# Kernel tuning notes

Hardware: AMD Instinct MI355X
Metric: run time of the kernel (lower is better)

Reference implementation:

```python
import jax, jax.numpy as jnp
import numpy as np

NB_STEPS = 300  # quadrature steps hard-coded in EmbeddingNet.__init__
B, D, C = 2048, 128, 64  # batch, in_main(=in_embedding), out_embedding


def _glorot(key, shape):
    fan_in, fan_out = shape
    lim = (6.0 / (fan_in + fan_out)) ** 0.5
    return jax.random.uniform(key, shape, jnp.float32, -lim, lim)


def setup_inputs() -> dict:
    key = jax.random.key(0)
    ks = jax.random.split(key, 9)
    x = jax.random.uniform(ks[0], (B, D), jnp.float32)
    # embedding net: D -> 200 -> 200 -> C (ReLU after every layer)
    W1 = _glorot(ks[1], (D, 200)); b1 = jnp.zeros((200,), jnp.float32)
    W2 = _glorot(ks[2], (200, 200)); b2 = jnp.zeros((200,), jnp.float32)
    W3 = _glorot(ks[3], (200, C)); b3 = jnp.zeros((C,), jnp.float32)
    # UMNN integrand net: (D + C) -> 100 -> 100 -> 100 -> D, positive output via ELU+1
    U1 = _glorot(ks[4], (D + C, 100)); c1 = jnp.zeros((100,), jnp.float32)
    U2 = _glorot(ks[5], (100, 100)); c2 = jnp.zeros((100,), jnp.float32)
    U3 = _glorot(ks[6], (100, 100)); c3 = jnp.zeros((100,), jnp.float32)
    U4 = _glorot(ks[7], (100, D)); c4 = jnp.zeros((D,), jnp.float32)
    return {"x": x, "W1": W1, "b1": b1, "W2": W2, "b2": b2, "W3": W3, "b3": b3,
            "U1": U1, "c1": c1, "U2": U2, "c2": c2, "U3": U3, "c3": c3,
            "U4": U4, "c4": c4}


def _forward(x, W1, b1, W2, b2, W3, b3, U1, c1, U2, c2, U3, c3, U4, c4):
    # conditioning embedding h = embedding_net(x)
    h = jax.nn.relu(x @ W1 + b1)
    h = jax.nn.relu(h @ W2 + b2)
    h = jax.nn.relu(h @ W3 + b3)                                   # (B, C)
    # UMNN: F(x,h) = int_0^1 f(t*x, h) . x dt, f > 0 via ELU+1 => monotone in each x_d.
    # All NB_STEPS quadrature points evaluated as one batched GEMM (the 'fast' form
    # of the original Python-level 300-step loop). Midpoint rule on (0,1).
    t = (jnp.arange(NB_STEPS, dtype=x.dtype) + 0.5) / NB_STEPS     # (T,)
    X = t[None, :, None] * x[:, None, :]                           # (B, T, D) points on path 0 -> x
    Hc = jnp.broadcast_to(h[:, None, :], (x.shape[0], NB_STEPS, h.shape[1]))
    z = jnp.concatenate([X, Hc], axis=-1)                          # (B, T, D+C)
    a = jax.nn.relu(z @ U1 + c1)
    a = jax.nn.relu(a @ U2 + c2)
    a = jax.nn.relu(a @ U3 + c3)
    f = jax.nn.elu(a @ U4 + c4) + 1.0                              # (B, T, D), strictly positive
    F = jnp.einsum('btd,bd->b', f, x) / NB_STEPS                   # line-integral quadrature
    return jax.nn.sigmoid(F)[:, None]                              # (B, 1)


def reference(x, W1, b1, W2, b2, W3, b3, U1, c1, U2, c2, U3, c3, U4, c4):
    return _forward(x, W1, b1, W2, b2, W3, b3, U1, c1, U2, c2, U3, c3, U4, c4)
```

## Files before the change

### kernel.cpp

```cpp
#include <hip/hip_runtime.h>

typedef __attribute__((ext_vector_type(8))) short bf16x8;
typedef __attribute__((ext_vector_type(4))) float f32x4;
typedef __attribute__((ext_vector_type(16))) float f32x16;
typedef int v2i __attribute__((ext_vector_type(2)));

union U4B { unsigned u[4]; bf16x8 v; };

__device__ __forceinline__ unsigned short f2bf(float f) {
    union { float f; unsigned u; } v; v.f = f;
    unsigned r = v.u + 0x7fffu + ((v.u >> 16) & 1u);
    return (unsigned short)(r >> 16);
}

__device__ __forceinline__ unsigned pkbf(float a, float b) {
    unsigned r;
    asm("v_cvt_pk_bf16_f32 %0, %1, %2" : "=v"(r) : "v"(a), "v"(b));
    return r;
}

__device__ __forceinline__ f32x16 zero16() {
    f32x16 v;
#pragma unroll
    for (int i = 0; i < 16; ++i) v[i] = 0.f;
    return v;
}

#define BATCH   2048
#define TSTEPS  300
#define ROWS_PB 4
#define WT_OFF  0
#define G_OFF   98304
#define E_OFF   1146880
#define OFF_X   98304
#define OFF_G   100352
#define OFF_E   102400
#define OFF_P   104448
#define SMEM_SZ 104480

__global__ __launch_bounds__(256) void prep_kernel(
    const float* __restrict__ U2, const float* __restrict__ c2,
    const float* __restrict__ U3, const float* __restrict__ c3,
    const float* __restrict__ U4, const float* __restrict__ c4,
    unsigned char* __restrict__ ws)
{
    int idx = blockIdx.x * 256 + threadIdx.x;
    for (int i = idx; i < 3 * 128 * 128; i += 48 * 256) {
        int m = i >> 14;
        int r = i & 16383;
        int n = r >> 7;
        int k = r & 127;
        float v = 0.f;
        if (m == 2) {
            if (k < 100)       v = U4[k * 128 + n];
            else if (k == 100) v = c4[n];
        } else {
            const float* U = (m == 0) ? U2 : U3;
            const float* c = (m == 0) ? c2 : c3;
            if (n < 100) {
                if (k < 100)       v = U[k * 100 + n];
                else if (k == 100) v = c[n];
            } else if (n == 100 && k == 100) {
                v = 1.f;
            }
        }
        *(unsigned short*)(ws + WT_OFF + m * 32768 + n * 256 + k * 2) = f2bf(v);
    }
}

__global__ __launch_bounds__(256) void embed_kernel(
    const float* __restrict__ x,
    const float* __restrict__ W1, const float* __restrict__ b1,
    const float* __restrict__ W2, const float* __restrict__ b2,
    const float* __restrict__ W3, const float* __restrict__ b3,
    const float* __restrict__ U1, const float* __restrict__ c1,
    float* __restrict__ g_out, float* __restrict__ e_out)
{
    __shared__ float xs[4][128];
    __shared__ float h1[4][200];
    __shared__ float h2[4][200];
    __shared__ float h3[4][64];
    const int tid = threadIdx.x;
    const int b0 = blockIdx.x * 4;

    for (int i = tid; i < 4 * 128; i += 256) {
        int r = i >> 7, d = i & 127;
        xs[r][d] = x[(b0 + r) * 128 + d];
    }
    __syncthreads();

    const int j = tid;
    if (j < 200) {
        float acc[4];
#pragma unroll
        for (int r = 0; r < 4; ++r) acc[r] = b1[j];
        for (int d = 0; d < 128; ++d) {
            float w = W1[d * 200 + j];
#pragma unroll
            for (int r = 0; r < 4; ++r) acc[r] += xs[r][d] * w;
        }
#pragma unroll
        for (int r = 0; r < 4; ++r) h1[r][j] = fmaxf(acc[r], 0.f);
    }
    __syncthreads();
    if (j < 200) {
        float acc[4];
#pragma unroll
        for (int r = 0; r < 4; ++r) acc[r] = b2[j];
        for (int d = 0; d < 200; ++d) {
            float w = W2[d * 200 + j];
#pragma unroll
            for (int r = 0; r < 4; ++r) acc[r] += h1[r][d] * w;
        }
#pragma unroll
        for (int r = 0; r < 4; ++r) h2[r][j] = fmaxf(acc[r], 0.f);
    }
    __syncthreads();
    if (j < 64) {
        float acc[4];
#pragma unroll
        for (int r = 0; r < 4; ++r) acc[r] = b3[j];
        for (int d = 0; d < 200; ++d) {
            float w = W3[d * 64 + j];
#pragma unroll
            for (int r = 0; r < 4; ++r) acc[r] += h2[r][d] * w;
        }
#pragma unroll
        for (int r = 0; r < 4; ++r) h3[r][j] = fmaxf(acc[r], 0.f);
    }
    __syncthreads();
    if (j < 128) {
        float ga[4], ea[4];
#pragma unroll
        for (int r = 0; r < 4; ++r) { ga[r] = 0.f; ea[r] = 0.f; }
        if (j < 100) {
            for (int d = 0; d < 128; ++d) {
                float w = U1[d * 100 + j];
#pragma unroll
                for (int r = 0; r < 4; ++r) ga[r] += xs[r][d] * w;
            }
#pragma unroll
            for (int r = 0; r < 4; ++r) ea[r] = c1[j];
            for (int c = 0; c < 64; ++c) {
                float w = U1[(128 + c) * 100 + j];
#pragma unroll
                for (int r = 0; r < 4; ++r) ea[r] += h3[r][c] * w;
            }
        } else if (j == 100) {
#pragma unroll
            for (int r = 0; r < 4; ++r) ea[r] = 1.f;
        }
#pragma unroll
        for (int r = 0; r < 4; ++r) {
            g_out[(b0 + r) * 128 + j] = ga[r];
            e_out[(b0 + r) * 128 + j] = ea[r];
        }
    }
}

__global__ __launch_bounds__(512, 1) void umnn_main(
    const float* __restrict__ x,
    const float* __restrict__ ws_g, const float* __restrict__ ws_e,
    const unsigned char* __restrict__ ws, float* __restrict__ out)
{
    extern __shared__ char sm[];
    float* sX = (float*)(sm + OFF_X);
    float* sG = (float*)(sm + OFF_G);
    float* sE = (float*)(sm + OFF_E);
    float* sP = (float*)(sm + OFF_P);
    const int tid = threadIdx.x;
    const int lane = tid & 63, wid = tid >> 6;
    const int l31 = lane & 31, hi = lane >> 5;
    const int b4 = blockIdx.x * ROWS_PB;

    {
        const uint4* src = (const uint4*)(ws + WT_OFF);
        for (int ci = tid; ci < 6144; ci += 512) {
            int m = ci >> 11, wi = ci & 2047, n = wi >> 4, part = wi & 15;
            uint4 v = src[ci];
            *(uint4*)(sm + m * 32768 + n * 256 + ((part * 16) ^ ((n & 7) << 4))) = v;
        }
        {
            int i = tid;
            int r = i >> 7, d = i & 127;
            sX[i] = x[(b4 + r) * 128 + d];
            sG[i] = ws_g[(b4 + r) * 128 + d];
            sE[i] = ws_e[(b4 + r) * 128 + d];
        }
    }
    __syncthreads();

    const int row = wid >> 1, half = wid & 1;
    const float* gR = sG + row * 128;
    const float* eR = sE + row * 128;
    const float* xR = sX + row * 128;
    const int sw = (l31 & 7) << 4;
    const char* wB2 = sm;
    const char* wB3 = sm + 32768;
    const char* wB4 = sm + 65536;

    float sumF = 0.f;

#pragma unroll 1
    for (int s = 0; s < 5; ++s) {
        const int t = half * 160 + s * 32 + l31;
        const float tt = ((float)t + 0.5f) * (1.f / 300.f);

        bf16x8 B[7];
#pragma unroll
        for (int ks = 0; ks < 7; ++ks) {
            const int k0 = ks * 16 + hi * 8;
            f32x4 g0 = *(const f32x4*)(gR + k0);
            f32x4 g1 = *(const f32x4*)(gR + k0 + 4);
            f32x4 e0 = *(const f32x4*)(eR + k0);
            f32x4 e1 = *(const f32x4*)(eR + k0 + 4);
            float a0 = fmaxf(fmaf(tt, g0[0], e0[0]), 0.f);
            float a1 = fmaxf(fmaf(tt, g0[1], e0[1]), 0.f);
            float a2 = fmaxf(fmaf(tt, g0[2], e0[2]), 0.f);
            float a3 = fmaxf(fmaf(tt, g0[3], e0[3]), 0.f);
            float a4 = fmaxf(fmaf(tt, g1[0], e1[0]), 0.f);
            float a5 = fmaxf(fmaf(tt, g1[1], e1[1]), 0.f);
            float a6 = fmaxf(fmaf(tt, g1[2], e1[2]), 0.f);
            float a7 = fmaxf(fmaf(tt, g1[3], e1[3]), 0.f);
            U4B u;
            u.u[0] = pkbf(a0, a1); u.u[1] = pkbf(a2, a3);
            u.u[2] = pkbf(a4, a5); u.u[3] = pkbf(a6, a7);
            B[ks] = u.v;
        }

#pragma unroll
        for (int L = 0; L < 2; ++L) {
            const char* wb = (L == 0) ? wB2 : wB3;
            f32x16 acc[4];
#pragma unroll
            for (int f = 0; f < 4; ++f) acc[f] = zero16();
#pragma unroll
            for (int ks = 0; ks < 7; ++ks) {
                const int ko = ks * 32 + hi * 16;
#pragma unroll
                for (int f = 0; f < 4; ++f) {
                    bf16x8 a = *(const bf16x8*)(wb + (32 * f + l31) * 256 + (ko ^ sw));
                    acc[f] = __builtin_amdgcn_mfma_f32_32x32x16_bf16(a, B[ks], acc[f], 0, 0, 0);
                }
            }
#pragma unroll
            for (int f = 0; f < 4; ++f) {
#pragma unroll
                for (int r = 0; r < 16; ++r) acc[f][r] = fmaxf(acc[f][r], 0.f);
                {
                    unsigned u  = pkbf(acc[f][0], acc[f][1]);
                    unsigned u2 = pkbf(acc[f][2], acc[f][3]);
                    unsigned v  = pkbf(acc[f][4], acc[f][5]);
                    unsigned v2 = pkbf(acc[f][6], acc[f][7]);
                    v2i r1 = __builtin_amdgcn_permlane32_swap(u, v, false, false);
                    v2i r2 = __builtin_amdgcn_permlane32_swap(u2, v2, false, false);
                    U4B b; b.u[0] = r1.x; b.u[1] = r2.x; b.u[2] = r1.y; b.u[3] = r2.y;
                    B[2 * f] = b.v;
                }
                if (f < 3) {
                    unsigned u  = pkbf(acc[f][8],  acc[f][9]);
                    unsigned u2 = pkbf(acc[f][10], acc[f][11]);
                    unsigned v  = pkbf(acc[f][12], acc[f][13]);
                    unsigned v2 = pkbf(acc[f][14], acc[f][15]);
                    v2i r1 = __builtin_amdgcn_permlane32_swap(u, v, false, false);
                    v2i r2 = __builtin_amdgcn_permlane32_swap(u2, v2, false, false);
                    U4B b; b.u[0] = r1.x; b.u[1] = r2.x; b.u[2] = r1.y; b.u[3] = r2.y;
                    B[2 * f + 1] = b.v;
                }
            }
        }

        float sdot = 0.f;
#pragma unroll
        for (int f = 0; f < 4; ++f) {
            f32x16 acc = zero16();
#pragma unroll
            for (int ks = 0; ks < 7; ++ks) {
                const int ko = ks * 32 + hi * 16;
                bf16x8 a = *(const bf16x8*)(wB4 + (32 * f + l31) * 256 + (ko ^ sw));
                acc = __builtin_amdgcn_mfma_f32_32x32x16_bf16(a, B[ks], acc, 0, 0, 0);
            }
#pragma unroll
            for (int q = 0; q < 4; ++q) {
                const int n0 = f * 32 + q * 8 + hi * 4;
                f32x4 xv = *(const f32x4*)(xR + n0);
#pragma unroll
                for (int i = 0; i < 4; ++i) {
                    float p = acc[q * 4 + i];
                    float fv = (p > 0.f) ? (p + 1.f) : __expf(p);
                    sdot = fmaf(fv, xv[i], sdot);
                }
            }
        }
        if (t < TSTEPS) sumF += sdot;
    }

#pragma unroll
    for (int off = 32; off >= 1; off >>= 1) sumF += __shfl_xor(sumF, off);
    if (lane == 0) sP[wid] = sumF;
    __syncthreads();
    if (tid < ROWS_PB) {
        float F = (sP[tid * 2] + sP[tid * 2 + 1]) * (1.f / 300.f);
        out[b4 + tid] = 1.f / (1.f + __expf(-F));
    }
}

extern "C" void kernel_launch(void* const* d_in, const int* in_sizes, int n_in,
                              void* d_out, int out_size, void* d_ws, size_t ws_size,
                              hipStream_t stream)
{
    const float* x  = (const float*)d_in[0];
    const float* W1 = (const float*)d_in[1];
    const float* b1 = (const float*)d_in[2];
    const float* W2 = (const float*)d_in[3];
    const float* b2 = (const float*)d_in[4];
    const float* W3 = (const float*)d_in[5];
    const float* b3 = (const float*)d_in[6];
    const float* U1 = (const float*)d_in[7];
    const float* c1 = (const float*)d_in[8];
    const float* U2 = (const float*)d_in[9];
    const float* c2 = (const float*)d_in[10];
    const float* U3 = (const float*)d_in[11];
    const float* c3 = (const float*)d_in[12];
    const float* U4 = (const float*)d_in[13];
    const float* c4 = (const float*)d_in[14];
    float* out = (float*)d_out;
    unsigned char* ws = (unsigned char*)d_ws;

    prep_kernel<<<48, 256, 0, stream>>>(U2, c2, U3, c3, U4, c4, ws);
    embed_kernel<<<BATCH / 4, 256, 0, stream>>>(x, W1, b1, W2, b2, W3, b3, U1, c1,
                                                (float*)(ws + G_OFF), (float*)(ws + E_OFF));
    hipFuncSetAttribute((const void*)umnn_main,
                        hipFuncAttributeMaxDynamicSharedMemorySize, SMEM_SZ);
    umnn_main<<<BATCH / ROWS_PB, 512, SMEM_SZ, stream>>>(
        x, (const float*)(ws + G_OFF), (const float*)(ws + E_OFF), ws, out);
}
```

Baseline: 168.3 us.

## Move embedding net to bf16 MFMA and process eight rows per main block

Replaces the scalar per-row embedding kernel with a 16-block MFMA version. It stages bf16 swizzled weights in LDS, runs all four small GEMMs on matrix cores, and writes g/e as bf16. The main UMNN kernel now handles 8 batch rows per 1024-thread block, so each LDS weight load is shared by more rows, and it uses a wider XOR swizzle. Risks: the embedding runs on only 16 blocks, bf16 intermediates lose precision, and launch_bounds(1024,2) may force a low VGPR budget and cause spills.

New measurement: 240.2 us. 42.7% more time.

```diff
diff --git a/kernel.cpp b/kernel.cpp
--- a/kernel.cpp
+++ b/kernel.cpp
@@ -12,13 +12,24 @@
     unsigned r = v.u + 0x7fffu + ((v.u >> 16) & 1u);
     return (unsigned short)(r >> 16);
 }
-
+__device__ __forceinline__ float bf2f(unsigned short s) {
+    union { unsigned u; float f; } v; v.u = ((unsigned)s) << 16; return v.f;
+}
 __device__ __forceinline__ unsigned pkbf(float a, float b) {
     unsigned r;
     asm("v_cvt_pk_bf16_f32 %0, %1, %2" : "=v"(r) : "v"(a), "v"(b));
     return r;
 }
-
+__device__ __forceinline__ bf16x8 packhalf(const f32x16& a, int base) {
+    unsigned u  = pkbf(a[base + 0], a[base + 1]);
+    unsigned u2 = pkbf(a[base + 2], a[base + 3]);
+    unsigned v  = pkbf(a[base + 4], a[base + 5]);
+    unsigned v2 = pkbf(a[base + 6], a[base + 7]);
+    v2i r1 = __builtin_amdgcn_permlane32_swap(u, v, false, false);
+    v2i r2 = __builtin_amdgcn_permlane32_swap(u2, v2, false, false);
+    U4B b; b.u[0] = r1.x; b.u[1] = r2.x; b.u[2] = r1.y; b.u[3] = r2.y;
+    return b.v;
+}
 __device__ __forceinline__ f32x16 zero16() {
     f32x16 v;
 #pragma unroll
@@ -28,15 +39,20 @@
 
 #define BATCH   2048
 #define TSTEPS  300
-#define ROWS_PB 4
-#define WT_OFF  0
+#define ROWS_PB 8
+#define WM_OFF  0
 #define G_OFF   98304
-#define E_OFF   1146880
+#define E_OFF   622592
 #define OFF_X   98304
-#define OFF_G   100352
-#define OFF_E   102400
-#define OFF_P   104448
-#define SMEM_SZ 104480
+#define OFF_G   102400
+#define OFF_E   106496
+#define OFF_P   110592
+#define SMEM_M  110656
+#define EB1     114688
+#define EB2     115584
+#define EB3     116480
+#define EC1     116736
+#define SMEM_E  117248
 
 __global__ __launch_bounds__(256) void prep_kernel(
     const float* __restrict__ U2, const float* __restrict__ c2,
@@ -45,7 +61,7 @@
     unsigned char* __restrict__ ws)
 {
     int idx = blockIdx.x * 256 + threadIdx.x;
-    for (int i = idx; i < 3 * 128 * 128; i += 48 * 256) {
+    for (int i = idx; i < 3 * 128 * 128; i += 24 * 256) {
         int m = i >> 14;
         int r = i & 16383;
         int n = r >> 7;
@@ -64,103 +80,202 @@
                 v = 1.f;
             }
         }
-        *(unsigned short*)(ws + WT_OFF + m * 32768 + n * 256 + k * 2) = f2bf(v);
-    }
-}
-
-__global__ __launch_bounds__(256) void embed_kernel(
+        *(unsigned short*)(ws + WM_OFF + m * 32768 + n * 256 + k * 2) = f2bf(v);
+    }
+}
+
+__global__ __launch_bounds__(256, 1) void embed2(
     const float* __restrict__ x,
     const float* __restrict__ W1, const float* __restrict__ b1,
     const float* __restrict__ W2, const float* __restrict__ b2,
     const float* __restrict__ W3, const float* __restrict__ b3,
     const float* __restrict__ U1, const float* __restrict__ c1,
-    float* __restrict__ g_out, float* __restrict__ e_out)
+    unsigned char* __restrict__ ws)
 {
-    __shared__ float xs[4][128];
-    __shared__ float h1[4][200];
-    __shared__ float h2[4][200];
-    __shared__ float h3[4][64];
+    extern __shared__ char sm[];
     const int tid = threadIdx.x;
-    const int b0 = blockIdx.x * 4;
-
-    for (int i = tid; i < 4 * 128; i += 256) {
-        int r = i >> 7, d = i & 127;
-        xs[r][d] = x[(b0 + r) * 128 + d];
-    }
-    __syncthreads();
-
-    const int j = tid;
-    if (j < 200) {
-        float acc[4];
-#pragma unroll
-        for (int r = 0; r < 4; ++r) acc[r] = b1[j];
-        for (int d = 0; d < 128; ++d) {
-            float w = W1[d * 200 + j];
-#pragma unroll
-            for (int r = 0; r < 4; ++r) acc[r] += xs[r][d] * w;
-        }
-#pragma unroll
-        for (int r = 0; r < 4; ++r) h1[r][j] = fmaxf(acc[r], 0.f);
-    }
-    __syncthreads();
-    if (j < 200) {
-        float acc[4];
-#pragma unroll
-        for (int r = 0; r < 4; ++r) acc[r] = b2[j];
-        for (int d = 0; d < 200; ++d) {
-            float w = W2[d * 200 + j];
-#pragma unroll
-            for (int r = 0; r < 4; ++r) acc[r] += h1[r][d] * w;
-        }
-#pragma unroll
-        for (int r = 0; r < 4; ++r) h2[r][j] = fmaxf(acc[r], 0.f);
-    }
-    __syncthreads();
-    if (j < 64) {
-        float acc[4];
-#pragma unroll
-        for (int r = 0; r < 4; ++r) acc[r] = b3[j];
-        for (int d = 0; d < 200; ++d) {
-            float w = W3[d * 64 + j];
-#pragma unroll
-            for (int r = 0; r < 4; ++r) acc[r] += h2[r][d] * w;
-        }
-#pragma unroll
-        for (int r = 0; r < 4; ++r) h3[r][j] = fmaxf(acc[r], 0.f);
-    }
-    __syncthreads();
-    if (j < 128) {
-        float ga[4], ea[4];
-#pragma unroll
-        for (int r = 0; r < 4; ++r) { ga[r] = 0.f; ea[r] = 0.f; }
-        if (j < 100) {
-            for (int d = 0; d < 128; ++d) {
-                float w = U1[d * 100 + j];
-#pragma unroll
-                for (int r = 0; r < 4; ++r) ga[r] += xs[r][d] * w;
-            }
-#pragma unroll
-            for (int r = 0; r < 4; ++r) ea[r] = c1[j];
-            for (int c = 0; c < 64; ++c) {
-                float w = U1[(128 + c) * 100 + j];
-#pragma unroll
-                for (int r = 0; r < 4; ++r) ea[r] += h3[r][c] * w;
-            }
-        } else if (j == 100) {
-#pragma unroll
-            for (int r = 0; r < 4; ++r) ea[r] = 1.f;
-        }
-#pragma unroll
-        for (int r = 0; r < 4; ++r) {
-            g_out[(b0 + r) * 128 + j] = ga[r];
-            e_out[(b0 + r) * 128 + j] = ea[r];
-        }
-    }
-}
-
-__global__ __launch_bounds__(512, 1) void umnn_main(
+    const int lane = tid & 63, wid = tid >> 6;
+    const int l31 = lane & 31, hi = lane >> 5;
+    const int brow = blockIdx.x * 128 + wid * 32 + l31;
+    const int sw8 = (l31 & 15) << 4;
+    const int sw9 = (l31 & 31) << 4;
+
+    for (int i = tid; i < 224; i += 256) ((float*)(sm + EB1))[i] = (i < 200) ? b1[i] : 0.f;
+    for (int i = tid; i < 224; i += 256) ((float*)(sm + EB2))[i] = (i < 200) ? b2[i] : 0.f;
+    if (tid < 64)  ((float*)(sm + EB3))[tid] = b3[tid];
+    if (tid < 128) ((float*)(sm + EC1))[tid] = (tid < 100) ? c1[tid] : 0.f;
+
+    for (int i = tid; i < 224 * 128; i += 256) {
+        int n = i >> 7, k = i & 127;
+        float v = (n < 200) ? W1[k * 200 + n] : 0.f;
+        *(unsigned short*)(sm + n * 256 + ((k * 2) ^ ((n & 15) << 4))) = f2bf(v);
+    }
+    for (int i = tid; i < 128 * 128; i += 256) {
+        int n = i >> 7, k = i & 127;
+        float v = (n < 100) ? U1[k * 100 + n] : 0.f;
+        *(unsigned short*)(sm + 57344 + n * 256 + ((k * 2) ^ ((n & 15) << 4))) = f2bf(v);
+    }
+    __syncthreads();
+
+    bf16x8 Bx[8];
+    {
+        const float* xr = x + brow * 128;
+#pragma unroll
+        for (int ks = 0; ks < 8; ++ks) {
+            const int k0 = ks * 16 + hi * 8;
+            f32x4 a = *(const f32x4*)(xr + k0);
+            f32x4 b = *(const f32x4*)(xr + k0 + 4);
+            U4B u;
+            u.u[0] = pkbf(a[0], a[1]); u.u[1] = pkbf(a[2], a[3]);
+            u.u[2] = pkbf(b[0], b[1]); u.u[3] = pkbf(b[2], b[3]);
+            Bx[ks] = u.v;
+        }
+    }
+
+    unsigned short* g16 = (unsigned short*)(ws + G_OFF);
+    unsigned short* e16 = (unsigned short*)(ws + E_OFF);
+
+    {
+        f32x16 ag[4];
+#pragma unroll
+        for (int f = 0; f < 4; ++f) ag[f] = zero16();
+#pragma unroll
+        for (int ks = 0; ks < 8; ++ks)
+#pragma unroll
+            for (int f = 0; f < 4; ++f) {
+                bf16x8 a = *(const bf16x8*)(sm + 57344 + (32 * f + l31) * 256 + ((ks * 32 + hi * 16) ^ sw8));
+                ag[f] = __builtin_amdgcn_mfma_f32_32x32x16_bf16(a, Bx[ks], ag[f], 0, 0, 0);
+            }
+#pragma unroll
+        for (int f = 0; f < 4; ++f)
+#pragma unroll
+            for (int r = 0; r < 16; r += 2) {
+                int n = 32 * f + (r & 3) + 8 * (r >> 2) + 4 * hi;
+                *(unsigned*)(g16 + brow * 128 + n) = pkbf(ag[f][r], ag[f][r + 1]);
+            }
+    }
+
+    bf16x8 Bh[13];
+    {
+        f32x16 acc[7];
+#pragma unroll
+        for (int f = 0; f < 7; ++f)
+#pragma unroll
+            for (int r = 0; r < 16; ++r)
+                acc[f][r] = ((float*)(sm + EB1))[32 * f + (r & 3) + 8 * (r >> 2) + 4 * hi];
+#pragma unroll
+        for (int ks = 0; ks < 8; ++ks)
+#pragma unroll
+            for (int f = 0; f < 7; ++f) {
+                bf16x8 a = *(const bf16x8*)(sm + (32 * f + l31) * 256 + ((ks * 32 + hi * 16) ^ sw8));
+                acc[f] = __builtin_amdgcn_mfma_f32_32x32x16_bf16(a, Bx[ks], acc[f], 0, 0, 0);
+            }
+#pragma unroll
+        for (int f = 0; f < 7; ++f) {
+#pragma unroll
+            for (int r = 0; r < 16; ++r) acc[f][r] = fmaxf(acc[f][r], 0.f);
+            Bh[2 * f] = packhalf(acc[f], 0);
+            if (f < 6) Bh[2 * f + 1] = packhalf(acc[f], 8);
+        }
+    }
+    __syncthreads();
+
+    for (int i = tid; i < 224 * 256; i += 256) {
+        int n = i >> 8, k = i & 255;
+        float v = (n < 200 && k < 200) ? W2[k * 200 + n] : 0.f;
+        *(unsigned short*)(sm + n * 512 + ((k * 2) ^ ((n & 31) << 4))) = f2bf(v);
+    }
+    __syncthreads();
+
+    bf16x8 Bh2[13];
+    {
+        f32x16 acc[7];
+#pragma unroll
+        for (int f = 0; f < 7; ++f)
+#pragma unroll
+            for (int r = 0; r < 16; ++r)
+                acc[f][r] = ((float*)(sm + EB2))[32 * f + (r & 3) + 8 * (r >> 2) + 4 * hi];
+#pragma unroll
+        for (int ks = 0; ks < 13; ++ks)
+#pragma unroll
+            for (int f = 0; f < 7; ++f) {
+                bf16x8 a = *(const bf16x8*)(sm + (32 * f + l31) * 512 + ((ks * 32 + hi * 16) ^ sw9));
+                acc[f] = __builtin_amdgcn_mfma_f32_32x32x16_bf16(a, Bh[ks], acc[f], 0, 0, 0);
+            }
+#pragma unroll
+        for (int f = 0; f < 7; ++f) {
+#pragma unroll
+            for (int r = 0; r < 16; ++r) acc[f][r] = fmaxf(acc[f][r], 0.f);
+            Bh2[2 * f] = packhalf(acc[f], 0);
+            if (f < 6) Bh2[2 * f + 1] = packhalf(acc[f], 8);
+        }
+    }
+    __syncthreads();
+
+    for (int i = tid; i < 64 * 256; i += 256) {
+        int n = i >> 8, k = i & 255;
+        float v = (k < 200) ? W3[k * 64 + n] : 0.f;
+        *(unsigned short*)(sm + n * 512 + ((k * 2) ^ ((n & 31) << 4))) = f2bf(v);
+    }
+    for (int i = tid; i < 128 * 128; i += 256) {
+        int n = i >> 7, k = i & 127;
+        float v = (n < 100 && k < 64) ? U1[(128 + k) * 100 + n] : 0.f;
+        *(unsigned short*)(sm + 32768 + n * 256 + ((k * 2) ^ ((n & 15) << 4))) = f2bf(v);
+    }
+    __syncthreads();
+
+    bf16x8 B4[4];
+    {
+        f32x16 acc[2];
+#pragma unroll
+        for (int f = 0; f < 2; ++f)
+#pragma unroll
+            for (int r = 0; r < 16; ++r)
+                acc[f][r] = ((float*)(sm + EB3))[32 * f + (r & 3) + 8 * (r >> 2) + 4 * hi];
+#pragma unroll
+        for (int ks = 0; ks < 13; ++ks)
+#pragma unroll
+            for (int f = 0; f < 2; ++f) {
+                bf16x8 a = *(const bf16x8*)(sm + (32 * f + l31) * 512 + ((ks * 32 + hi * 16) ^ sw9));
+                acc[f] = __builtin_amdgcn_mfma_f32_32x32x16_bf16(a, Bh2[ks], acc[f], 0, 0, 0);
+            }
+#pragma unroll
+        for (int f = 0; f < 2; ++f) {
+#pragma unroll
+            for (int r = 0; r < 16; ++r) acc[f][r] = fmaxf(acc[f][r], 0.f);
+            B4[2 * f]     = packhalf(acc[f], 0);
+            B4[2 * f + 1] = packhalf(acc[f], 8);
+        }
+    }
+
+    {
+        f32x16 ae[4];
+#pragma unroll
+        for (int f = 0; f < 4; ++f)
+#pragma unroll
+            for (int r = 0; r < 16; ++r)
+                ae[f][r] = ((float*)(sm + EC1))[32 * f + (r & 3) + 8 * (r >> 2) + 4 * hi];
+#pragma unroll
+        for (int ks = 0; ks < 4; ++ks)
+#pragma unroll
+            for (int f = 0; f < 4; ++f) {
+                bf16x8 a = *(const bf16x8*)(sm + 32768 + (32 * f + l31) * 256 + ((ks * 32 + hi * 16) ^ sw8));
+                ae[f] = __builtin_amdgcn_mfma_f32_32x32x16_bf16(a, B4[ks], ae[f], 0, 0, 0);
+            }
+#pragma unroll
+        for (int f = 0; f < 4; ++f)
+#pragma unroll
+            for (int r = 0; r < 16; r += 2) {
+                int n = 32 * f + (r & 3) + 8 * (r >> 2) + 4 * hi;
+                float v0 = ae[f][r], v1 = ae[f][r + 1];
+                if (n == 100) v0 = 1.f;
+                *(unsigned*)(e16 + brow * 128 + n) = pkbf(v0, v1);
+            }
+    }
+}
+
+__global__ __launch_bounds__(1024, 2) void umnn_main(
     const float* __restrict__ x,
-    const float* __restrict__ ws_g, const float* __restrict__ ws_e,
     const unsigned char* __restrict__ ws, float* __restrict__ out)
 {
     extern __shared__ char sm[];
@@ -171,21 +286,22 @@
     const int tid = threadIdx.x;
     const int lane = tid & 63, wid = tid >> 6;
     const int l31 = lane & 31, hi = lane >> 5;
-    const int b4 = blockIdx.x * ROWS_PB;
-
-    {
-        const uint4* src = (const uint4*)(ws + WT_OFF);
-        for (int ci = tid; ci < 6144; ci += 512) {
+    const int b8 = blockIdx.x * ROWS_PB;
+
+    {
+        const uint4* src = (const uint4*)(ws + WM_OFF);
+        for (int ci = tid; ci < 6144; ci += 1024) {
             int m = ci >> 11, wi = ci & 2047, n = wi >> 4, part = wi & 15;
             uint4 v = src[ci];
-            *(uint4*)(sm + m * 32768 + n * 256 + ((part * 16) ^ ((n & 7) << 4))) = v;
-        }
+            *(uint4*)(sm + m * 32768 + n * 256 + ((part * 16) ^ ((n & 15) << 4))) = v;
+        }
+        const unsigned short* g16 = (const unsigned short*)(ws + G_OFF);
+        const unsigned short* e16 = (const unsigned short*)(ws + E_OFF);
         {
-            int i = tid;
-            int r = i >> 7, d = i & 127;
-            sX[i] = x[(b4 + r) * 128 + d];
-            sG[i] = ws_g[(b4 + r) * 128 + d];
-            sE[i] = ws_e[(b4 + r) * 128 + d];
+            int r = tid >> 7, d = tid & 127;
+            sX[tid] = x[(b8 + r) * 128 + d];
+            sG[tid] = bf2f(g16[(b8 + r) * 128 + d]);
+            sE[tid] = bf2f(e16[(b8 + r) * 128 + d]);
         }
     }
     __syncthreads();
@@ -194,7 +310,7 @@
     const float* gR = sG + row * 128;
     const float* eR = sE + row * 128;
     const float* xR = sX + row * 128;
-    const int sw = (l31 & 7) << 4;
+    const int sw = (l31 & 15) << 4;
     const char* wB2 = sm;
     const char* wB3 = sm + 32768;
     const char* wB4 = sm + 65536;
@@ -247,26 +363,8 @@
             for (int f = 0; f < 4; ++f) {
 #pragma unroll
                 for (int r = 0; r < 16; ++r) acc[f][r] = fmaxf(acc[f][r], 0.f);
-                {
-                    unsigned u  = pkbf(acc[f][0], acc[f][1]);
-                    unsigned u2 = pkbf(acc[f][2], acc[f][3]);
-                    unsigned v  = pkbf(acc[f][4], acc[f][5]);
-                    unsigned v2 = pkbf(acc[f][6], acc[f][7]);
-                    v2i r1 = __builtin_amdgcn_permlane32_swap(u, v, false, false);
-                    v2i r2 = __builtin_amdgcn_permlane32_swap(u2, v2, false, false);
-                    U4B b; b.u[0] = r1.x; b.u[1] = r2.x; b.u[2] = r1.y; b.u[3] = r2.y;
-                    B[2 * f] = b.v;
-                }
-                if (f < 3) {
-                    unsigned u  = pkbf(acc[f][8],  acc[f][9]);
-                    unsigned u2 = pkbf(acc[f][10], acc[f][11]);
-                    unsigned v  = pkbf(acc[f][12], acc[f][13]);
-                    unsigned v2 = pkbf(acc[f][14], acc[f][15]);
-                    v2i r1 = __builtin_amdgcn_permlane32_swap(u, v, false, false);
-                    v2i r2 = __builtin_amdgcn_permlane32_swap(u2, v2, false, false);
-                    U4B b; b.u[0] = r1.x; b.u[1] = r2.x; b.u[2] = r1.y; b.u[3] = r2.y;
-                    B[2 * f + 1] = b.v;
-                }
+                B[2 * f] = packhalf(acc[f], 0);
+                if (f < 3) B[2 * f + 1] = packhalf(acc[f], 8);
             }
         }
 
@@ -301,7 +399,7 @@
     __syncthreads();
     if (tid < ROWS_PB) {
         float F = (sP[tid * 2] + sP[tid * 2 + 1]) * (1.f / 300.f);
-        out[b4 + tid] = 1.f / (1.f + __expf(-F));
+        out[b8 + tid] = 1.f / (1.f + __expf(-F));
     }
 }
 
@@ -327,11 +425,11 @@
     float* out = (float*)d_out;
     unsigned char* ws = (unsigned char*)d_ws;
 
-    prep_kernel<<<48, 256, 0, stream>>>(U2, c2, U3, c3, U4, c4, ws);
-    embed_kernel<<<BATCH / 4, 256, 0, stream>>>(x, W1, b1, W2, b2, W3, b3, U1, c1,
-                                                (float*)(ws + G_OFF), (float*)(ws + E_OFF));
+    prep_kernel<<<24, 256, 0, stream>>>(U2, c2, U3, c3, U4, c4, ws);
+    hipFuncSetAttribute((const void*)embed2,
+                        hipFuncAttributeMaxDynamicSharedMemorySize, SMEM_E);
+    embed2<<<16, 256, SMEM_E, stream>>>(x, W1, b1, W2, b2, W3, b3, U1, c1, ws);
     hipFuncSetAttribute((const void*)umnn_main,
-                        hipFuncAttributeMaxDynamicSharedMemorySize, SMEM_SZ);
-    umnn_main<<<BATCH / ROWS_PB, 512, SMEM_SZ, stream>>>(
-        x, (const float*)(ws + G_OFF), (const float*)(ws + E_OFF), ws, out);
-}
+                        hipFuncAttributeMaxDynamicSharedMemorySize, SMEM_M);
+    umnn_main<<<BATCH / ROWS_PB, 1024, SMEM_M, stream>>>(x, ws, out);
+}
```
